# Kernel optimization log

Hardware: AMD Instinct MI355X
Metric: run time of the kernel (lower is better)

The kernel has to match this reference:

```python
import jax, jax.numpy as jnp
import numpy as np

NUM_USERS = 100000
NUM_ITEMS = 50000
EMBED_DIM = 64
N_LAYERS = 3
NUM_EDGES = 3276800  # avg user degree 32
BATCH = 16384


def setup_inputs() -> dict:
    key = jax.random.key(0)
    k0, k1, k2, k3, k4, k5 = jax.random.split(key, 6)
    rows = jax.random.randint(k0, (NUM_EDGES,), 0, NUM_USERS, dtype=jnp.int32)
    cols = jax.random.randint(k1, (NUM_EDGES,), 0, NUM_ITEMS, dtype=jnp.int32)
    user_table = jax.random.normal(k2, (NUM_USERS, EMBED_DIM), dtype=jnp.float32) * 0.1
    item_table = jax.random.normal(k3, (NUM_ITEMS, EMBED_DIM), dtype=jnp.float32) * 0.1
    user_indices = jax.random.randint(k4, (BATCH,), 0, NUM_USERS, dtype=jnp.int32)
    item_indices = jax.random.randint(k5, (BATCH,), 0, NUM_ITEMS, dtype=jnp.int32)
    return {
        "user_table": user_table,
        "item_table": item_table,
        "rows": rows,
        "cols": cols,
        "user_indices": user_indices,
        "item_indices": item_indices,
    }


def reference(user_table, item_table, rows, cols, user_indices, item_indices):
    # D^-1 A row-normalization of the binary bipartite adjacency:
    # normalized edge value for edge (u, i) is 1 / deg(u) (0 if isolated).
    ones = jnp.ones(rows.shape, dtype=user_table.dtype)
    deg = jax.ops.segment_sum(ones, rows, num_segments=NUM_USERS)
    inv_deg = jnp.where(deg > 0, 1.0 / deg, 0.0)
    vals = inv_deg[rows]  # [E]

    u = user_table  # [U, D] (unused by propagation in the original too)
    it = item_table  # [I, D]
    for _ in range(N_LAYERS):
        # u = A @ it  (SpMM via gather + segment-sum over destination users)
        u = jax.ops.segment_sum(vals[:, None] * it[cols], rows, num_segments=NUM_USERS)
        # it = A^T @ u
        it = jax.ops.segment_sum(vals[:, None] * u[rows], cols, num_segments=NUM_ITEMS)

    scores = jnp.sum(u[user_indices] * it[item_indices], axis=-1)  # [B]
    return jax.nn.sigmoid(scores)
```

## Files before the change

kernel.cpp:

```cpp
#include <hip/hip_runtime.h>
#include <math.h>

#define NUM_USERS 100000
#define NUM_ITEMS 50000
#define EMBED     64
#define NUM_EDGES 3276800
#define BATCH     16384
#define CAP       12800
#define NBUCK     391
#define P1_EDGES  8192
#define P1_THREADS 512
#define P2_THREADS 1024
#define CVT_BLOCKS 1563

typedef _Float16 half8 __attribute__((ext_vector_type(8)));

__global__ void prep_kernel(const float* __restrict__ itab, _Float16* __restrict__ it16,
                            int* __restrict__ curzero, _Float16* __restrict__ w16) {
    int b = blockIdx.x;
    if (b < CVT_BLOCKS) {
        int i = b * 256 + threadIdx.x;
        if (i < NUM_ITEMS * EMBED / 8) {
            const float4* p = (const float4*)itab + 2 * i;
            float4 a = p[0], c = p[1];
            half8 o;
            o[0] = (_Float16)a.x; o[1] = (_Float16)a.y; o[2] = (_Float16)a.z; o[3] = (_Float16)a.w;
            o[4] = (_Float16)c.x; o[5] = (_Float16)c.y; o[6] = (_Float16)c.z; o[7] = (_Float16)c.w;
            ((half8*)it16)[i] = o;
        }
    } else if (b == CVT_BLOCKS) {
        for (int k = threadIdx.x; k < 800; k += 256) curzero[k] = 0;
    } else {
        int i = threadIdx.x;
        if (i < 64) w16[(long long)NUM_USERS * EMBED + i] = (_Float16)0.f;
        else if (i < 128) it16[(long long)NUM_ITEMS * EMBED + (i - 64)] = (_Float16)0.f;
    }
}

__global__ void __launch_bounds__(P1_THREADS)
pass1_kernel(const int* __restrict__ rows, const int* __restrict__ cols,
             int* __restrict__ ucur, int* __restrict__ icur,
             int* __restrict__ rec_u, int* __restrict__ rec_i) {
    __shared__ int hu[400], hi[400], gu[400], gi[400];
    __shared__ int lbase[400], lcur[400];
    __shared__ int sc[512];
    __shared__ int recbuf[P1_EDGES];
    int t = threadIdx.x;
    long long e0 = (long long)blockIdx.x * P1_EDGES;

    int er[16], ec[16];
    #pragma unroll
    for (int q = 0; q < 16; ++q) {
        er[q] = rows[e0 + t + q * P1_THREADS];
        ec[q] = cols[e0 + t + q * P1_THREADS];
    }

    for (int i = t; i < 400; i += P1_THREADS) { hu[i] = 0; hi[i] = 0; }
    __syncthreads();
    #pragma unroll
    for (int q = 0; q < 16; ++q) {
        atomicAdd(&hu[er[q] >> 8], 1);
        atomicAdd(&hi[ec[q] >> 7], 1);
    }
    __syncthreads();
    for (int i = t; i < 400; i += P1_THREADS) {
        int vr = (hu[i] + 15) & ~15;
        gu[i] = vr ? atomicAdd(&ucur[i], vr) : 0;
        vr = (hi[i] + 15) & ~15;
        gi[i] = vr ? atomicAdd(&icur[i], vr) : 0;
    }

    __syncthreads();
    sc[t] = (t < 400) ? hu[t] : 0;
    __syncthreads();
    for (int o = 1; o < 512; o <<= 1) {
        int x = (t >= o) ? sc[t - o] : 0; __syncthreads();
        sc[t] += x; __syncthreads();
    }
    if (t < 400) { lbase[t] = sc[t] - hu[t]; lcur[t] = 0; }
    __syncthreads();
    #pragma unroll
    for (int q = 0; q < 16; ++q) {
        int b = er[q] >> 8;
        int p = lbase[b] + atomicAdd(&lcur[b], 1);
        recbuf[p] = (ec[q] << 8) | (er[q] & 255);
    }
    __syncthreads();
    sc[t] = (t < 400) ? ((hu[t] + 15) & ~15) : 0;
    __syncthreads();
    for (int o = 1; o < 512; o <<= 1) {
        int x = (t >= o) ? sc[t - o] : 0; __syncthreads();
        sc[t] += x; __syncthreads();
    }
    int total = sc[511];
    for (int o4 = t * 4; o4 < total; o4 += P1_THREADS * 4) {
        int lo = 0, hi_ = 399;
        while (lo < hi_) { int mid = (lo + hi_) >> 1; if (sc[mid] > o4) hi_ = mid; else lo = mid + 1; }
        int b = lo;
        int v = hu[b];
        int vr = (v + 15) & ~15;
        int j = o4 - (sc[b] - vr);
        int gpos = gu[b] + j;
        if (gpos + 3 < CAP) {
            int4 val;
            val.x = (j + 0 < v) ? recbuf[lbase[b] + j + 0] : -1;
            val.y = (j + 1 < v) ? recbuf[lbase[b] + j + 1] : -1;
            val.z = (j + 2 < v) ? recbuf[lbase[b] + j + 2] : -1;
            val.w = (j + 3 < v) ? recbuf[lbase[b] + j + 3] : -1;
            *(int4*)(rec_u + (long long)b * CAP + gpos) = val;
        } else {
            for (int k = 0; k < 4; ++k)
                if (gpos + k < CAP)
                    rec_u[(long long)b * CAP + gpos + k] = (j + k < v) ? recbuf[lbase[b] + j + k] : -1;
        }
    }

    __syncthreads();
    sc[t] = (t < 400) ? hi[t] : 0;
    __syncthreads();
    for (int o = 1; o < 512; o <<= 1) {
        int x = (t >= o) ? sc[t - o] : 0; __syncthreads();
        sc[t] += x; __syncthreads();
    }
    if (t < 400) { lbase[t] = sc[t] - hi[t]; lcur[t] = 0; }
    __syncthreads();
    #pragma unroll
    for (int q = 0; q < 16; ++q) {
        int b = ec[q] >> 7;
        int p = lbase[b] + atomicAdd(&lcur[b], 1);
        recbuf[p] = (er[q] << 7) | (ec[q] & 127);
    }
    __syncthreads();
    sc[t] = (t < 400) ? ((hi[t] + 15) & ~15) : 0;
    __syncthreads();
    for (int o = 1; o < 512; o <<= 1) {
        int x = (t >= o) ? sc[t - o] : 0; __syncthreads();
        sc[t] += x; __syncthreads();
    }
    total = sc[511];
    for (int o4 = t * 4; o4 < total; o4 += P1_THREADS * 4) {
        int lo = 0, hi_ = 399;
        while (lo < hi_) { int mid = (lo + hi_) >> 1; if (sc[mid] > o4) hi_ = mid; else lo = mid + 1; }
        int b = lo;
        int v = hi[b];
        int vr = (v + 15) & ~15;
        int j = o4 - (sc[b] - vr);
        int gpos = gi[b] + j;
        if (gpos + 3 < CAP) {
            int4 val;
            val.x = (j + 0 < v) ? recbuf[lbase[b] + j + 0] : -1;
            val.y = (j + 1 < v) ? recbuf[lbase[b] + j + 1] : -1;
            val.z = (j + 2 < v) ? recbuf[lbase[b] + j + 2] : -1;
            val.w = (j + 3 < v) ? recbuf[lbase[b] + j + 3] : -1;
            *(int4*)(rec_i + (long long)b * CAP + gpos) = val;
        } else {
            for (int k = 0; k < 4; ++k)
                if (gpos + k < CAP)
                    rec_i[(long long)b * CAP + gpos + k] = (j + k < v) ? recbuf[lbase[b] + j + k] : -1;
        }
    }
}

template <int VBITS>
__device__ __forceinline__ void pass2_body(int* __restrict__ rec, const int* __restrict__ cur,
                                           int* __restrict__ deg, int* __restrict__ off,
                                           float* __restrict__ inv32, int ncap, int b,
                                           int* buf, int* h, int* ex, int* cnt, int* sc) {
    const int V = 1 << VBITS, M = V - 1;
    int t = threadIdx.x;
    long long s = (long long)b * CAP;
    int n = cur[b]; if (n > CAP) n = CAP;
    int nv = (n + 3) >> 2;
    const int4* rec4 = (const int4*)(rec + s);
    for (int i = t; i < nv; i += P2_THREADS) {
        int4 v4 = rec4[i];
        buf[4 * i + 0] = v4.x; buf[4 * i + 1] = v4.y;
        buf[4 * i + 2] = v4.z; buf[4 * i + 3] = v4.w;
    }
    if (t < V) { h[t] = 0; cnt[t] = 0; }
    __syncthreads();
    for (int i = t; i < n; i += P2_THREADS) {
        int r = buf[i];
        if (r != -1) atomicAdd(&h[r & M], 1);
    }
    __syncthreads();
    if (t < V) sc[t] = h[t];
    __syncthreads();
    for (int o = 1; o < V; o <<= 1) {
        int x = (t >= o && t < V) ? sc[t - o] : 0;
        __syncthreads();
        if (t < V) sc[t] += x;
        __syncthreads();
    }
    if (t < V) {
        ex[t] = sc[t] - h[t];
        int id = b * V + t;
        if (id < ncap) {
            int v = h[t];
            deg[id] = v;
            off[id] = (int)(s + ex[t]);
            if (inv32) inv32[id] = v ? 1.0f / (float)v : 0.0f;
        }
    }
    __syncthreads();
    for (int i = t; i < n; i += P2_THREADS) {
        int r = buf[i];
        if (r == -1) continue;
        int k = r & M;
        int rnk = atomicAdd(&cnt[k], 1);
        rec[s + ex[k] + rnk] = (int)(((unsigned)r) >> VBITS);
    }
}

__global__ void __launch_bounds__(P2_THREADS)
pass2_kernel(int* __restrict__ rec_u, const int* __restrict__ ucur,
             int* __restrict__ udeg, int* __restrict__ uoff, float* __restrict__ inv32,
             int* __restrict__ rec_i, const int* __restrict__ icur,
             int* __restrict__ ideg, int* __restrict__ ioff) {
    __shared__ int buf[CAP];
    __shared__ int h[256], ex[256], cnt[256], sc[256];
    if (blockIdx.x < NBUCK)
        pass2_body<8>(rec_u, ucur, udeg, uoff, inv32, NUM_USERS, blockIdx.x,
                      buf, h, ex, cnt, sc);
    else
        pass2_body<7>(rec_i, icur, ideg, ioff, (float*)nullptr, NUM_ITEMS,
                      blockIdx.x - NBUCK, buf, h, ex, cnt, sc);
}

__global__ void gather_u(const int* __restrict__ uoff, const int* __restrict__ udeg,
                         const int* __restrict__ csr_col, const float* __restrict__ inv32,
                         const _Float16* __restrict__ it, _Float16* __restrict__ w) {
    int row = blockIdx.x * 4 + (threadIdx.x >> 6);
    if (row >= NUM_USERS) return;
    int lane = threadIdx.x & 63;
    int slot = lane >> 3;
    int h    = lane & 7;
    int start = uoff[row];
    int end = start + udeg[row];
    half8 acc = {0, 0, 0, 0, 0, 0, 0, 0};
    for (int k = start; k < end; k += 64) {
        int e1 = end - 1;
        int idx[8], c[8];
        #pragma unroll
        for (int q = 0; q < 8; ++q) {
            idx[q] = k + slot + q * 8;
            int safe = idx[q] < e1 ? idx[q] : e1;
            c[q] = csr_col[safe];
            c[q] = idx[q] < end ? c[q] : NUM_ITEMS;
        }
        half8 x[8];
        #pragma unroll
        for (int q = 0; q < 8; ++q)
            x[q] = *(const half8*)(it + (long long)c[q] * EMBED + (h << 3));
        #pragma unroll
        for (int q = 0; q < 8; ++q) acc += x[q];
    }
    float f[8];
    #pragma unroll
    for (int j = 0; j < 8; ++j) {
        f[j] = (float)acc[j];
        f[j] += __shfl_xor(f[j], 8, 64);
        f[j] += __shfl_xor(f[j], 16, 64);
        f[j] += __shfl_xor(f[j], 32, 64);
    }
    if (lane < 8) {
        float v = inv32[row];
        float v2 = v * v;
        half8 ow;
        #pragma unroll
        for (int j = 0; j < 8; ++j) ow[j] = (_Float16)(f[j] * v2);
        *(half8*)(w + (long long)row * EMBED + (lane << 3)) = ow;
    }
}

__global__ void gather_it(const int* __restrict__ ioff, const int* __restrict__ ideg,
                          const int* __restrict__ csc_row,
                          const _Float16* __restrict__ w, _Float16* __restrict__ it) {
    int col = blockIdx.x * 4 + (threadIdx.x >> 6);
    if (col >= NUM_ITEMS) return;
    int lane = threadIdx.x & 63;
    int slot = lane >> 3;
    int h    = lane & 7;
    int start = ioff[col];
    int end = start + ideg[col];
    half8 acc = {0, 0, 0, 0, 0, 0, 0, 0};
    for (int k = start; k < end; k += 64) {
        int e1 = end - 1;
        int idx[8], r[8];
        #pragma unroll
        for (int q = 0; q < 8; ++q) {
            idx[q] = k + slot + q * 8;
            int safe = idx[q] < e1 ? idx[q] : e1;
            r[q] = csc_row[safe];
            r[q] = idx[q] < end ? r[q] : NUM_USERS;
        }
        half8 x[8];
        #pragma unroll
        for (int q = 0; q < 8; ++q)
            x[q] = *(const half8*)(w + (long long)r[q] * EMBED + (h << 3));
        #pragma unroll
        for (int q = 0; q < 8; ++q) acc += x[q];
    }
    float f[8];
    #pragma unroll
    for (int j = 0; j < 8; ++j) {
        f[j] = (float)acc[j];
        f[j] += __shfl_xor(f[j], 8, 64);
        f[j] += __shfl_xor(f[j], 16, 64);
        f[j] += __shfl_xor(f[j], 32, 64);
    }
    if (lane < 8) {
        half8 o;
        #pragma unroll
        for (int j = 0; j < 8; ++j) o[j] = (_Float16)f[j];
        *(half8*)(it + (long long)col * EMBED + (lane << 3)) = o;
    }
}

__global__ void batch_score(const int* __restrict__ ioff, const int* __restrict__ ideg,
                            const int* __restrict__ csc_row, const _Float16* __restrict__ w,
                            const int* __restrict__ udeg,
                            const int* __restrict__ uidx, const int* __restrict__ iidx,
                            float* __restrict__ out) {
    int b = blockIdx.x * 4 + (threadIdx.x >> 6);
    if (b >= BATCH) return;
    int lane = threadIdx.x & 63;
    int col = iidx[b];
    int slot = lane >> 3;
    int h    = lane & 7;
    int start = ioff[col];
    int end = start + ideg[col];
    half8 acc = {0, 0, 0, 0, 0, 0, 0, 0};
    for (int k = start; k < end; k += 64) {
        int e1 = end - 1;
        int idx[8], r[8];
        #pragma unroll
        for (int q = 0; q < 8; ++q) {
            idx[q] = k + slot + q * 8;
            int safe = idx[q] < e1 ? idx[q] : e1;
            r[q] = csc_row[safe];
            r[q] = idx[q] < end ? r[q] : NUM_USERS;
        }
        half8 x[8];
        #pragma unroll
        for (int q = 0; q < 8; ++q)
            x[q] = *(const half8*)(w + (long long)r[q] * EMBED + (h << 3));
        #pragma unroll
        for (int q = 0; q < 8; ++q) acc += x[q];
    }
    float f[8];
    #pragma unroll
    for (int j = 0; j < 8; ++j) {
        f[j] = (float)acc[j];
        f[j] += __shfl_xor(f[j], 8, 64);
        f[j] += __shfl_xor(f[j], 16, 64);
        f[j] += __shfl_xor(f[j], 32, 64);
    }
    int ui = uidx[b];
    half8 wv = *(const half8*)(w + (long long)ui * EMBED + (h << 3));
    float p = 0.f;
    #pragma unroll
    for (int j = 0; j < 8; ++j) p += f[j] * (float)wv[j];
    p += __shfl_xor(p, 1, 64);
    p += __shfl_xor(p, 2, 64);
    p += __shfl_xor(p, 4, 64);
    if (lane == 0) {
        float s = p * (float)udeg[ui];
        out[b] = 1.0f / (1.0f + expf(-s));
    }
}

extern "C" void kernel_launch(void* const* d_in, const int* in_sizes, int n_in,
                              void* d_out, int out_size, void* d_ws, size_t ws_size,
                              hipStream_t stream) {
    const float* item_table = (const float*)d_in[1];
    const int*   rows       = (const int*)d_in[2];
    const int*   cols       = (const int*)d_in[3];
    const int*   uidx       = (const int*)d_in[4];
    const int*   iidx       = (const int*)d_in[5];
    float* out = (float*)d_out;

    char* base = (char*)d_ws;
    int*   udeg  = (int*)(base + 0);
    int*   ideg  = (int*)(base +   400000);
    int*   uoff  = (int*)(base +   600000);
    int*   ioff  = (int*)(base +  1000000);
    float* inv32 = (float*)(base + 1200000);
    int*   ucur  = (int*)(base +  1600000);
    int*   icur  = (int*)(base +  1601600);
    int*   rec_u = (int*)(base +  1720320);
    int*   rec_i = (int*)(base + 22200320);
    _Float16* w16  = (_Float16*)(base + 42680320);
    _Float16* it16 = (_Float16*)(base + 55480448);

    prep_kernel<<<CVT_BLOCKS + 2, 256, 0, stream>>>(item_table, it16, ucur, w16);

    pass1_kernel<<<NUM_EDGES / P1_EDGES, P1_THREADS, 0, stream>>>(
        rows, cols, ucur, icur, rec_u, rec_i);
    pass2_kernel<<<NBUCK * 2, P2_THREADS, 0, stream>>>(rec_u, ucur, udeg, uoff, inv32,
                                                       rec_i, icur, ideg, ioff);

    const int ublocks = (NUM_USERS + 3) / 4;
    const int iblocks = (NUM_ITEMS + 3) / 4;
    for (int l = 0; l < 3; ++l) {
        gather_u<<<ublocks, 256, 0, stream>>>(uoff, udeg, rec_u, inv32, it16, w16);
        if (l < 2)
            gather_it<<<iblocks, 256, 0, stream>>>(ioff, ideg, rec_i, w16, it16);
    }
    batch_score<<<BATCH / 4, 256, 0, stream>>>(ioff, ideg, rec_i, w16, udeg,
                                               uidx, iidx, out);
}
```

Baseline: 413.1 us.

## Pad CSR/CSC segments to multiples of 32 with sentinels to remove bounds checks

Pass2 now rounds each row/column segment length up to a multiple of 32 and fills the padding slots with a sentinel index that points at the zero row. The gather kernels can then loop over the padded length with 32-edge steps and no per-element bounds clamping or masking. In exchange, bucket capacity and workspace grow, and the padding adds wasted gathers, about 16 per row on average against degrees near 32 for users and 64 for items.

Result: slower. 547.0 us (+32.4%).

```diff
diff --git a/kernel.cpp b/kernel.cpp
--- a/kernel.cpp
+++ b/kernel.cpp
@@ -6,7 +6,7 @@
 #define EMBED     64
 #define NUM_EDGES 3276800
 #define BATCH     16384
-#define CAP       12800
+#define CAP       13824
 #define NBUCK     391
 #define P1_EDGES  8192
 #define P1_THREADS 512
@@ -163,8 +163,9 @@
 
 template <int VBITS>
 __device__ __forceinline__ void pass2_body(int* __restrict__ rec, const int* __restrict__ cur,
-                                           int* __restrict__ deg, int* __restrict__ off,
-                                           float* __restrict__ inv32, int ncap, int b,
+                                           int* __restrict__ rdeg, int* __restrict__ pdeg,
+                                           int* __restrict__ off, float* __restrict__ inv32,
+                                           int ncap, int sentinel, int b,
                                            int* buf, int* h, int* ex, int* cnt, int* sc) {
     const int V = 1 << VBITS, M = V - 1;
     int t = threadIdx.x;
@@ -184,7 +185,7 @@
         if (r != -1) atomicAdd(&h[r & M], 1);
     }
     __syncthreads();
-    if (t < V) sc[t] = h[t];
+    if (t < V) sc[t] = (h[t] + 31) & ~31;
     __syncthreads();
     for (int o = 1; o < V; o <<= 1) {
         int x = (t >= o && t < V) ? sc[t - o] : 0;
@@ -193,11 +194,13 @@
         __syncthreads();
     }
     if (t < V) {
-        ex[t] = sc[t] - h[t];
+        int hpv = (h[t] + 31) & ~31;
+        ex[t] = sc[t] - hpv;
         int id = b * V + t;
         if (id < ncap) {
             int v = h[t];
-            deg[id] = v;
+            rdeg[id] = v;
+            pdeg[id] = hpv;
             off[id] = (int)(s + ex[t]);
             if (inv32) inv32[id] = v ? 1.0f / (float)v : 0.0f;
         }
@@ -210,24 +213,32 @@
         int rnk = atomicAdd(&cnt[k], 1);
         rec[s + ex[k] + rnk] = (int)(((unsigned)r) >> VBITS);
     }
+    __syncthreads();
+    if (t < V) {
+        int basep = (int)(s + ex[t]);
+        int v = h[t];
+        int hpv = (v + 31) & ~31;
+        for (int j = v; j < hpv; ++j) rec[basep + j] = sentinel;
+    }
 }
 
 __global__ void __launch_bounds__(P2_THREADS)
 pass2_kernel(int* __restrict__ rec_u, const int* __restrict__ ucur,
-             int* __restrict__ udeg, int* __restrict__ uoff, float* __restrict__ inv32,
+             int* __restrict__ udeg, int* __restrict__ updeg,
+             int* __restrict__ uoff, float* __restrict__ inv32,
              int* __restrict__ rec_i, const int* __restrict__ icur,
-             int* __restrict__ ideg, int* __restrict__ ioff) {
+             int* __restrict__ ideg, int* __restrict__ ipdeg, int* __restrict__ ioff) {
     __shared__ int buf[CAP];
     __shared__ int h[256], ex[256], cnt[256], sc[256];
     if (blockIdx.x < NBUCK)
-        pass2_body<8>(rec_u, ucur, udeg, uoff, inv32, NUM_USERS, blockIdx.x,
-                      buf, h, ex, cnt, sc);
+        pass2_body<8>(rec_u, ucur, udeg, updeg, uoff, inv32, NUM_USERS, NUM_ITEMS,
+                      blockIdx.x, buf, h, ex, cnt, sc);
     else
-        pass2_body<7>(rec_i, icur, ideg, ioff, (float*)nullptr, NUM_ITEMS,
+        pass2_body<7>(rec_i, icur, ideg, ipdeg, ioff, (float*)nullptr, NUM_ITEMS, NUM_USERS,
                       blockIdx.x - NBUCK, buf, h, ex, cnt, sc);
 }
 
-__global__ void gather_u(const int* __restrict__ uoff, const int* __restrict__ udeg,
+__global__ void gather_u(const int* __restrict__ uoff, const int* __restrict__ updeg,
                          const int* __restrict__ csr_col, const float* __restrict__ inv32,
                          const _Float16* __restrict__ it, _Float16* __restrict__ w) {
     int row = blockIdx.x * 4 + (threadIdx.x >> 6);
@@ -236,24 +247,18 @@
     int slot = lane >> 3;
     int h    = lane & 7;
     int start = uoff[row];
-    int end = start + udeg[row];
+    int pend = start + updeg[row];
     half8 acc = {0, 0, 0, 0, 0, 0, 0, 0};
-    for (int k = start; k < end; k += 64) {
-        int e1 = end - 1;
-        int idx[8], c[8];
-        #pragma unroll
-        for (int q = 0; q < 8; ++q) {
-            idx[q] = k + slot + q * 8;
-            int safe = idx[q] < e1 ? idx[q] : e1;
-            c[q] = csr_col[safe];
-            c[q] = idx[q] < end ? c[q] : NUM_ITEMS;
-        }
-        half8 x[8];
-        #pragma unroll
-        for (int q = 0; q < 8; ++q)
-            x[q] = *(const half8*)(it + (long long)c[q] * EMBED + (h << 3));
-        #pragma unroll
-        for (int q = 0; q < 8; ++q) acc += x[q];
+    for (int k = start; k < pend; k += 32) {
+        int c0 = csr_col[k + slot];
+        int c1 = csr_col[k + slot + 8];
+        int c2 = csr_col[k + slot + 16];
+        int c3 = csr_col[k + slot + 24];
+        half8 x0 = *(const half8*)(it + (long long)c0 * EMBED + (h << 3));
+        half8 x1 = *(const half8*)(it + (long long)c1 * EMBED + (h << 3));
+        half8 x2 = *(const half8*)(it + (long long)c2 * EMBED + (h << 3));
+        half8 x3 = *(const half8*)(it + (long long)c3 * EMBED + (h << 3));
+        acc += x0; acc += x1; acc += x2; acc += x3;
     }
     float f[8];
     #pragma unroll
@@ -273,7 +278,7 @@
     }
 }
 
-__global__ void gather_it(const int* __restrict__ ioff, const int* __restrict__ ideg,
+__global__ void gather_it(const int* __restrict__ ioff, const int* __restrict__ ipdeg,
                           const int* __restrict__ csc_row,
                           const _Float16* __restrict__ w, _Float16* __restrict__ it) {
     int col = blockIdx.x * 4 + (threadIdx.x >> 6);
@@ -282,24 +287,18 @@
     int slot = lane >> 3;
     int h    = lane & 7;
     int start = ioff[col];
-    int end = start + ideg[col];
+    int pend = start + ipdeg[col];
     half8 acc = {0, 0, 0, 0, 0, 0, 0, 0};
-    for (int k = start; k < end; k += 64) {
-        int e1 = end - 1;
-        int idx[8], r[8];
-        #pragma unroll
-        for (int q = 0; q < 8; ++q) {
-            idx[q] = k + slot + q * 8;
-            int safe = idx[q] < e1 ? idx[q] : e1;
-            r[q] = csc_row[safe];
-            r[q] = idx[q] < end ? r[q] : NUM_USERS;
-        }
-        half8 x[8];
-        #pragma unroll
-        for (int q = 0; q < 8; ++q)
-            x[q] = *(const half8*)(w + (long long)r[q] * EMBED + (h << 3));
-        #pragma unroll
-        for (int q = 0; q < 8; ++q) acc += x[q];
+    for (int k = start; k < pend; k += 32) {
+        int r0 = csc_row[k + slot];
+        int r1 = csc_row[k + slot + 8];
+        int r2 = csc_row[k + slot + 16];
+        int r3 = csc_row[k + slot + 24];
+        half8 x0 = *(const half8*)(w + (long long)r0 * EMBED + (h << 3));
+        half8 x1 = *(const half8*)(w + (long long)r1 * EMBED + (h << 3));
+        half8 x2 = *(const half8*)(w + (long long)r2 * EMBED + (h << 3));
+        half8 x3 = *(const half8*)(w + (long long)r3 * EMBED + (h << 3));
+        acc += x0; acc += x1; acc += x2; acc += x3;
     }
     float f[8];
     #pragma unroll
@@ -317,7 +316,7 @@
     }
 }
 
-__global__ void batch_score(const int* __restrict__ ioff, const int* __restrict__ ideg,
+__global__ void batch_score(const int* __restrict__ ioff, const int* __restrict__ ipdeg,
                             const int* __restrict__ csc_row, const _Float16* __restrict__ w,
                             const int* __restrict__ udeg,
                             const int* __restrict__ uidx, const int* __restrict__ iidx,
@@ -329,24 +328,18 @@
     int slot = lane >> 3;
     int h    = lane & 7;
     int start = ioff[col];
-    int end = start + ideg[col];
+    int pend = start + ipdeg[col];
     half8 acc = {0, 0, 0, 0, 0, 0, 0, 0};
-    for (int k = start; k < end; k += 64) {
-        int e1 = end - 1;
-        int idx[8], r[8];
-        #pragma unroll
-        for (int q = 0; q < 8; ++q) {
-            idx[q] = k + slot + q * 8;
-            int safe = idx[q] < e1 ? idx[q] : e1;
-            r[q] = csc_row[safe];
-            r[q] = idx[q] < end ? r[q] : NUM_USERS;
-        }
-        half8 x[8];
-        #pragma unroll
-        for (int q = 0; q < 8; ++q)
-            x[q] = *(const half8*)(w + (long long)r[q] * EMBED + (h << 3));
-        #pragma unroll
-        for (int q = 0; q < 8; ++q) acc += x[q];
+    for (int k = start; k < pend; k += 32) {
+        int r0 = csc_row[k + slot];
+        int r1 = csc_row[k + slot + 8];
+        int r2 = csc_row[k + slot + 16];
+        int r3 = csc_row[k + slot + 24];
+        half8 x0 = *(const half8*)(w + (long long)r0 * EMBED + (h << 3));
+        half8 x1 = *(const half8*)(w + (long long)r1 * EMBED + (h << 3));
+        half8 x2 = *(const half8*)(w + (long long)r2 * EMBED + (h << 3));
+        half8 x3 = *(const half8*)(w + (long long)r3 * EMBED + (h << 3));
+        acc += x0; acc += x1; acc += x2; acc += x3;
     }
     float f[8];
     #pragma unroll
@@ -386,27 +379,29 @@
     int*   uoff  = (int*)(base +   600000);
     int*   ioff  = (int*)(base +  1000000);
     float* inv32 = (float*)(base + 1200000);
-    int*   ucur  = (int*)(base +  1600000);
-    int*   icur  = (int*)(base +  1601600);
-    int*   rec_u = (int*)(base +  1720320);
-    int*   rec_i = (int*)(base + 22200320);
-    _Float16* w16  = (_Float16*)(base + 42680320);
-    _Float16* it16 = (_Float16*)(base + 55480448);
+    int*   updeg = (int*)(base +  1600000);
+    int*   ipdeg = (int*)(base +  2000000);
+    int*   ucur  = (int*)(base +  2200000);
+    int*   icur  = (int*)(base +  2201600);
+    int*   rec_u = (int*)(base +  2203200);
+    int*   rec_i = (int*)(base + 24321600);
+    _Float16* w16  = (_Float16*)(base + 46440000);
+    _Float16* it16 = (_Float16*)(base + 59240128);
 
     prep_kernel<<<CVT_BLOCKS + 2, 256, 0, stream>>>(item_table, it16, ucur, w16);
 
     pass1_kernel<<<NUM_EDGES / P1_EDGES, P1_THREADS, 0, stream>>>(
         rows, cols, ucur, icur, rec_u, rec_i);
-    pass2_kernel<<<NBUCK * 2, P2_THREADS, 0, stream>>>(rec_u, ucur, udeg, uoff, inv32,
-                                                       rec_i, icur, ideg, ioff);
+    pass2_kernel<<<NBUCK * 2, P2_THREADS, 0, stream>>>(rec_u, ucur, udeg, updeg, uoff, inv32,
+                                                       rec_i, icur, ideg, ipdeg, ioff);
 
     const int ublocks = (NUM_USERS + 3) / 4;
     const int iblocks = (NUM_ITEMS + 3) / 4;
     for (int l = 0; l < 3; ++l) {
-        gather_u<<<ublocks, 256, 0, stream>>>(uoff, udeg, rec_u, inv32, it16, w16);
+        gather_u<<<ublocks, 256, 0, stream>>>(uoff, updeg, rec_u, inv32, it16, w16);
         if (l < 2)
-            gather_it<<<iblocks, 256, 0, stream>>>(ioff, ideg, rec_i, w16, it16);
-    }
-    batch_score<<<BATCH / 4, 256, 0, stream>>>(ioff, ideg, rec_i, w16, udeg,
+            gather_it<<<iblocks, 256, 0, stream>>>(ioff, ipdeg, rec_i, w16, it16);
+    }
+    batch_score<<<BATCH / 4, 256, 0, stream>>>(ioff, ipdeg, rec_i, w16, udeg,
                                                uidx, iidx, out);
 }
```
